# Kernel tuning notes

Hardware: AMD Instinct MI355X
Metric: run time of the kernel (lower is better)

The kernel has to match this reference:

```python
import jax, jax.numpy as jnp
import numpy as np

B, S, D, H = 2, 2048, 1024, 16
DK = D // H

def setup_inputs() -> dict:
    key = jax.random.key(0)
    ks = jax.random.split(key, 12)
    sc = 0.02
    return {
        "q": jax.random.normal(ks[0], (B, S, D), jnp.float32),
        "k": jax.random.normal(ks[1], (B, S, D), jnp.float32),
        "v": jax.random.normal(ks[2], (B, S, D), jnp.float32),
        "mask": jnp.ones((1, 1, S, S), jnp.int32),
        "w_q": jax.random.normal(ks[3], (D, D), jnp.float32) * sc,
        "b_q": jnp.zeros((D,), jnp.float32),
        "w_k": jax.random.normal(ks[4], (D, D), jnp.float32) * sc,
        "b_k": jnp.zeros((D,), jnp.float32),
        "w_v": jax.random.normal(ks[5], (D, D), jnp.float32) * sc,
        "b_v": jnp.zeros((D,), jnp.float32),
        "w_o": jax.random.normal(ks[6], (D, D), jnp.float32) * sc,
        "b_o": jnp.zeros((D,), jnp.float32),
    }

def reference(q, k, v, mask, w_q, b_q, w_k, b_k, w_v, b_v, w_o, b_o):
    # torch Linear: y = x @ W.T + b, W is [out, in]
    def lin(x, w, b):
        return jnp.einsum('bsd,ed->bse', x, w) + b
    # project and split heads -> [B, H, S, DK]
    def heads(x):
        return x.reshape(B, S, H, DK).transpose(0, 2, 1, 3)
    Q = heads(lin(q, w_q, b_q))
    K = heads(lin(k, w_k, b_k))
    V = heads(lin(v, w_v, b_v))
    scores = jnp.einsum('bhqd,bhkd->bhqk', Q, K) / jnp.sqrt(jnp.float32(DK))
    scores = jnp.where(mask == 0, jnp.float32(-1e9), scores)
    attn = jax.nn.softmax(scores, axis=-1)  # dropout p=0 -> identity
    ctx = jnp.einsum('bhqk,bhkd->bhqd', attn, V)
    ctx = ctx.transpose(0, 2, 1, 3).reshape(B, S, D)
    return lin(ctx, w_o, b_o)
```

## Files before the change

### kernel.cpp

```cpp
#include <hip/hip_runtime.h>
#include <stdint.h>


#define S_LEN 2048
#define LOG2E 1.4426950408889634f

using bf16x8 = __attribute__((ext_vector_type(8))) __bf16;
using f32x4 = __attribute__((ext_vector_type(4))) float;
using f32x16 = __attribute__((ext_vector_type(16))) float;
using u32x4 = __attribute__((ext_vector_type(4))) unsigned int;

__device__ __forceinline__ unsigned short f2bf(float x) {
  unsigned int u = __builtin_bit_cast(unsigned int, x);
  u += 0x7fffu + ((u >> 16) & 1u);
  return (unsigned short)(u >> 16);
}

__device__ __forceinline__ float bf2f(unsigned short u) {
  unsigned int x = ((unsigned int)u) << 16;
  return __builtin_bit_cast(float, x);
}

__device__ __forceinline__ void gload_lds16(const void* g, void* l) {
  __builtin_amdgcn_global_load_lds(
      (const __attribute__((address_space(1))) void*)g,
      (__attribute__((address_space(3))) void*)l, 16, 0, 0);
}

__device__ __forceinline__ unsigned int cvtpk(float lo, float hi) {
  unsigned int r;
  asm("v_cvt_pk_bf16_f32 %0, %1, %2" : "=v"(r) : "v"(lo), "v"(hi));
  return r;
}

__device__ __forceinline__ bf16x8 mkfrag(float p0, float p1, float p2, float p3,
                                         float p4, float p5, float p6, float p7) {
  auto r02 = __builtin_amdgcn_permlane32_swap(cvtpk(p0, p1), cvtpk(p4, p5),
                                              false, false);
  auto r13 = __builtin_amdgcn_permlane32_swap(cvtpk(p2, p3), cvtpk(p6, p7),
                                              false, false);
  u32x4 w = {(unsigned int)r02[0], (unsigned int)r13[0], (unsigned int)r02[1],
             (unsigned int)r13[1]};
  return __builtin_bit_cast(bf16x8, w);
}

__global__ void cvt7_kernel(const float* __restrict__ q,
                            const float* __restrict__ k,
                            const float* __restrict__ v,
                            const float* __restrict__ w0,
                            const float* __restrict__ w1,
                            const float* __restrict__ w2,
                            const float* __restrict__ w3,
                            unsigned short* __restrict__ dq,
                            unsigned short* __restrict__ dk,
                            unsigned short* __restrict__ dv,
                            unsigned short* __restrict__ e0,
                            unsigned short* __restrict__ e1,
                            unsigned short* __restrict__ e2,
                            unsigned short* __restrict__ e3) {
  const int y = blockIdx.y;
  const float* src;
  unsigned short* dst;
  int n4;
  if (y < 3) {
    src = y == 0 ? q : y == 1 ? k : v;
    dst = y == 0 ? dq : y == 1 ? dk : dv;
    n4 = 1048576;
  } else {
    int j = y - 3;
    src = j == 0 ? w0 : j == 1 ? w1 : j == 2 ? w2 : w3;
    dst = j == 0 ? e0 : j == 1 ? e1 : j == 2 ? e2 : e3;
    n4 = 262144;
  }
  int i = blockIdx.x * blockDim.x + threadIdx.x;
  int stride = gridDim.x * blockDim.x;
  for (; i < n4; i += stride) {
    float4 a = ((const float4*)src)[i];
    ushort4 o;
    o.x = f2bf(a.x);
    o.y = f2bf(a.y);
    o.z = f2bf(a.z);
    o.w = f2bf(a.w);
    ((ushort4*)dst)[i] = o;
  }
}

template <int OMODE>
__device__ __forceinline__ void qkv128_body(
    unsigned short* As, unsigned short* Bs,
    const unsigned short* __restrict__ X, const unsigned short* __restrict__ W,
    const float* __restrict__ bias, unsigned short* __restrict__ dst,
    float scale, int tx, int ty) {
  const int tid = threadIdx.x;
  const int wid = tid >> 6, lane = tid & 63;
  const int l15 = lane & 15, lg = lane >> 4;
  const int bm = ty * 128, bn = tx * 128;
  const int wr = (wid >> 1) * 64, wc = (wid & 1) * 64;

  const f32x4 fz = {0.f, 0.f, 0.f, 0.f};
  f32x4 acc[4][4];
#pragma unroll
  for (int m = 0; m < 4; ++m)
#pragma unroll
    for (int n = 0; n < 4; ++n) acc[m][n] = fz;

  const int srow = lane >> 2;
  const int scolz = ((lane & 3) ^ ((lane >> 3) & 3)) * 8;
  const int rcol = (lg ^ ((l15 >> 1) & 3)) * 8;

  for (int kt = 0; kt < 1024; kt += 32) {
#pragma unroll
    for (int c = 0; c < 2; ++c) {
      int ch = wid * 2 + c;
      gload_lds16(X + (size_t)(bm + ch * 16 + srow) * 1024 + kt + scolz,
                  As + ch * 512);
      gload_lds16(W + (size_t)(bn + ch * 16 + srow) * 1024 + kt + scolz,
                  Bs + ch * 512);
    }
    __syncthreads();

    bf16x8 af[4], bf[4];
#pragma unroll
    for (int m = 0; m < 4; ++m)
      af[m] = *(const bf16x8*)&As[(wr + m * 16 + l15) * 32 + rcol];
#pragma unroll
    for (int n = 0; n < 4; ++n)
      bf[n] = *(const bf16x8*)&Bs[(wc + n * 16 + l15) * 32 + rcol];

#pragma unroll
    for (int m = 0; m < 4; ++m)
#pragma unroll
      for (int n = 0; n < 4; ++n) {
        if (OMODE == 2)
          acc[m][n] = __builtin_amdgcn_mfma_f32_16x16x32_bf16(bf[n], af[m],
                                                              acc[m][n], 0, 0, 0);
        else
          acc[m][n] = __builtin_amdgcn_mfma_f32_16x16x32_bf16(af[m], bf[n],
                                                              acc[m][n], 0, 0, 0);
      }
    __syncthreads();
  }

#pragma unroll
  for (int m = 0; m < 4; ++m)
#pragma unroll
    for (int n = 0; n < 4; ++n)
#pragma unroll
      for (int j = 0; j < 4; ++j) {
        float a = acc[m][n][j];
        if (OMODE == 2) {
          int gn = bn + wc + n * 16 + lg * 4 + j;
          int gm = bm + wr + m * 16 + l15;
          float v = a + bias[gn];
          int b = gm >> 11, s = gm & 2047;
          int h = gn >> 6, dk = gn & 63;
          dst[(((size_t)(b * 16 + h)) * 64 + dk) * 2048 + s] = f2bf(v);
        } else {
          int gm = bm + wr + m * 16 + lg * 4 + j;
          int gn = bn + wc + n * 16 + l15;
          float v = (a + bias[gn]) * scale;
          int b = gm >> 11, s = gm & 2047;
          int h = gn >> 6, dk = gn & 63;
          dst[(((size_t)(b * 16 + h)) * 2048 + s) * 64 + dk] = f2bf(v);
        }
      }
}

__global__ __launch_bounds__(256) void gemm_qkv(
    const unsigned short* __restrict__ X0, const unsigned short* __restrict__ X1,
    const unsigned short* __restrict__ X2, const unsigned short* __restrict__ W0,
    const unsigned short* __restrict__ W1,
    const unsigned short* __restrict__ W2, const float* __restrict__ b0,
    const float* __restrict__ b1, const float* __restrict__ b2,
    unsigned short* __restrict__ dq, unsigned short* __restrict__ dk,
    unsigned short* __restrict__ dv) {
  __shared__ unsigned short As[128 * 32];
  __shared__ unsigned short Bs[128 * 32];
  const int lin = blockIdx.x + 8 * (blockIdx.y + 32 * blockIdx.z);
  const int xcd = lin & 7, v = lin >> 3;
  const int panel = xcd * 12 + (v >> 3);
  const int tx = v & 7;
  const int z = panel >> 5, ty = panel & 31;
  if (z == 0)
    qkv128_body<0>(As, Bs, X0, W0, b0, dq, 0.125f * LOG2E, tx, ty);
  else if (z == 1)
    qkv128_body<0>(As, Bs, X1, W1, b1, dk, 1.0f, tx, ty);
  else
    qkv128_body<2>(As, Bs, X2, W2, b2, dv, 1.0f, tx, ty);
}

__global__ __launch_bounds__(256) void gemm_out(
    const unsigned short* __restrict__ X, const unsigned short* __restrict__ W,
    const float* __restrict__ bias, float* __restrict__ dstF) {
  const int lin = blockIdx.x + 8 * blockIdx.y;
  const int xcd = lin & 7, v = lin >> 3;
  const int ty = xcd * 8 + (v >> 3);
  const int tx = v & 7;

  __shared__ unsigned short As[3][64 * 32];
  __shared__ unsigned short Bs[3][128 * 32];
  const int tid = threadIdx.x;
  const int wid = tid >> 6, lane = tid & 63;
  const int l15 = lane & 15, lg = lane >> 4;
  const int bm = ty * 64, bn = tx * 128;
  const int wr = (wid >> 1) * 32, wc = (wid & 1) * 64;

  const f32x4 fz = {0.f, 0.f, 0.f, 0.f};
  f32x4 acc[2][4];
#pragma unroll
  for (int m = 0; m < 2; ++m)
#pragma unroll
    for (int n = 0; n < 4; ++n) acc[m][n] = fz;

  const int srow = lane >> 2;
  const int scolz = ((lane & 3) ^ ((lane >> 3) & 3)) * 8;
  const int rcol = (lg ^ ((l15 >> 1) & 3)) * 8;

#define GSTAGE(buf, kt)                                                       \
  {                                                                           \
    gload_lds16(X + (size_t)(bm + wid * 16 + srow) * 1024 + (kt) + scolz,     \
                &As[buf][wid * 512]);                                         \
    _Pragma("unroll") for (int c = 0; c < 2; ++c) {                           \
      int ch = wid * 2 + c;                                                   \
      gload_lds16(W + (size_t)(bn + ch * 16 + srow) * 1024 + (kt) + scolz,    \
                  &Bs[buf][ch * 512]);                                        \
    }                                                                         \
  }

  GSTAGE(0, 0)
  GSTAGE(1, 32)
  int cur = 0;

  for (int it = 0; it < 32; ++it) {
    if (it < 31) {
      asm volatile("s_waitcnt vmcnt(3)\n\ts_barrier" ::: "memory");
    } else {
      asm volatile("s_waitcnt vmcnt(0)\n\ts_barrier" ::: "memory");
    }
    if (it < 30) {
      int nb = cur >= 1 ? cur - 1 : cur + 2;
      GSTAGE(nb, (it + 2) * 32)
    }

    bf16x8 af[2], bf[4];
#pragma unroll
    for (int m = 0; m < 2; ++m)
      af[m] = *(const bf16x8*)&As[cur][(wr + m * 16 + l15) * 32 + rcol];
#pragma unroll
    for (int n = 0; n < 4; ++n)
      bf[n] = *(const bf16x8*)&Bs[cur][(wc + n * 16 + l15) * 32 + rcol];

#pragma unroll
    for (int m = 0; m < 2; ++m)
#pragma unroll
      for (int n = 0; n < 4; ++n)
        acc[m][n] = __builtin_amdgcn_mfma_f32_16x16x32_bf16(af[m], bf[n],
                                                            acc[m][n], 0, 0, 0);
    cur = cur == 2 ? 0 : cur + 1;
  }
#undef GSTAGE

#pragma unroll
  for (int m = 0; m < 2; ++m)
#pragma unroll
    for (int n = 0; n < 4; ++n)
#pragma unroll
      for (int j = 0; j < 4; ++j) {
        int gm = bm + wr + m * 16 + lg * 4 + j;
        int gn = bn + wc + n * 16 + l15;
        dstF[(size_t)gm * 1024 + gn] = acc[m][n][j] + bias[gn];
      }
}

__global__ __launch_bounds__(256) void attn_kernel(
    const unsigned short* __restrict__ Q,
    const unsigned short* __restrict__ K,
    const unsigned short* __restrict__ VT,
    unsigned short* __restrict__ Opart, float* __restrict__ lvec) {
  const int orig = blockIdx.x;
  const int idx = (orig & 7) * 128 + (orig >> 3);
  const int bh = idx >> 5;
  const int u = idx & 31;
  const int qb = u >> 1;
  const int sp = u & 1;
  const int kt0 = sp * 1024;
  const int tid = threadIdx.x;
  const int w = tid >> 6;
  const int lane = tid & 63;
  const int l31 = lane & 31;
  const int hi = lane >> 5;
  const int q0 = qb * 128 + w * 32;

  __shared__ __align__(16) unsigned short Ks[2][64][64];
  __shared__ __align__(16) unsigned short Vs[2][64][64];

  const unsigned short* Qg = Q + ((size_t)bh * S_LEN + q0) * 64;
  const unsigned short* Kg = K + (size_t)bh * S_LEN * 64;
  const unsigned short* Vg = VT + (size_t)bh * 64 * S_LEN;

  bf16x8 qf[4];
#pragma unroll
  for (int kc = 0; kc < 4; ++kc)
    qf[kc] = *(const bf16x8*)&Qg[l31 * 64 + kc * 16 + hi * 8];

  const u32x4 ow = {0x3F803F80u, 0x3F803F80u, 0x3F803F80u, 0x3F803F80u};
  const bf16x8 onesf = __builtin_bit_cast(bf16x8, ow);

  const int srow = lane >> 3;
  const int sslot = (lane & 7) ^ srow;

#define STAGE_K(buf, kt)                                                      \
  {                                                                           \
    gload_lds16(Kg + ((size_t)((kt) + w * 16 + srow)) * 64 + sslot * 8,       \
                &Ks[buf][w * 16][0]);                                         \
    gload_lds16(Kg + ((size_t)((kt) + w * 16 + 8 + srow)) * 64 + sslot * 8,   \
                &Ks[buf][w * 16 + 8][0]);                                     \
  }
#define STAGE_V(buf, kt)                                                       \
  {                                                                            \
    gload_lds16(Vg + ((size_t)(w * 16 + srow)) * S_LEN + (kt) + sslot * 8,     \
                &Vs[buf][w * 16][0]);                                          \
    gload_lds16(Vg + ((size_t)(w * 16 + 8 + srow)) * S_LEN + (kt) + sslot * 8, \
                &Vs[buf][w * 16 + 8][0]);                                      \
  }

  const f32x16 fz16 = {};
  f32x16 O0 = {}, O1 = {}, Lacc = {};
  f32x16 sA0, sA1, sB0, sB1;

  STAGE_K(0, kt0)
  STAGE_V(0, kt0)
  STAGE_K(1, kt0 + 64)
  asm volatile("s_waitcnt vmcnt(2)\n\ts_barrier" ::: "memory");
  sA0 = fz16;
  sA1 = fz16;
  __builtin_amdgcn_s_setprio(1);
#pragma unroll
  for (int kc = 0; kc < 4; ++kc) {
    const int col = ((kc * 2 + hi) ^ (l31 & 7)) * 8;
    bf16x8 kf0 = *(const bf16x8*)&Ks[0][l31][col];
    bf16x8 kf1 = *(const bf16x8*)&Ks[0][32 + l31][col];
    sA0 = __builtin_amdgcn_mfma_f32_32x32x16_bf16(kf0, qf[kc], sA0, 0, 0, 0);
    sA1 = __builtin_amdgcn_mfma_f32_32x32x16_bf16(kf1, qf[kc], sA1, 0, 0, 0);
  }
  __builtin_amdgcn_s_setprio(0);
  STAGE_V(1, kt0 + 64)

#define BODY(T, SP0, SP1, SN0, SN1, PB, DO_PRE, DO_QK)                         \
  {                                                                            \
    if (DO_QK) {                                                               \
      asm volatile("s_waitcnt vmcnt(2)\n\ts_barrier" ::: "memory");            \
    } else {                                                                   \
      asm volatile("s_waitcnt vmcnt(0)\n\ts_barrier" ::: "memory");            \
    }                                                                          \
    if (DO_PRE) STAGE_K(PB, kt0 + ((T) + 2) * 64)                              \
    if (DO_QK) {                                                               \
      SN0 = fz16;                                                              \
      SN1 = fz16;                                                              \
      __builtin_amdgcn_s_setprio(1);                                           \
      _Pragma("unroll") for (int kc = 0; kc < 4; ++kc) {                       \
        const int col = ((kc * 2 + hi) ^ (l31 & 7)) * 8;                       \
        bf16x8 kf0 = *(const bf16x8*)&Ks[1 - (PB)][l31][col];                  \
        bf16x8 kf1 = *(const bf16x8*)&Ks[1 - (PB)][32 + l31][col];             \
        SN0 =                                                                  \
            __builtin_amdgcn_mfma_f32_32x32x16_bf16(kf0, qf[kc], SN0, 0, 0, 0);\
        SN1 =                                                                  \
            __builtin_amdgcn_mfma_f32_32x32x16_bf16(kf1, qf[kc], SN1, 0, 0, 0);\
      }                                                                        \
      __builtin_amdgcn_s_setprio(0);                                           \
    }                                                                          \
    _Pragma("unroll") for (int r = 0; r < 16; ++r) {                           \
      SP0[r] = exp2f(SP0[r]);                                                  \
      SP1[r] = exp2f(SP1[r]);                                                  \
    }                                                                          \
    {                                                                          \
      bf16x8 pa0 = mkfrag(SP0[0], SP0[1], SP0[2], SP0[3], SP0[4], SP0[5],      \
                          SP0[6], SP0[7]);                                     \
      bf16x8 pa1 = mkfrag(SP0[8], SP0[9], SP0[10], SP0[11], SP0[12], SP0[13],  \
                          SP0[14], SP0[15]);                                   \
      bf16x8 pa2 = mkfrag(SP1[0], SP1[1], SP1[2], SP1[3], SP1[4], SP1[5],      \
                          SP1[6], SP1[7]);                                     \
      bf16x8 pa3 = mkfrag(SP1[8], SP1[9], SP1[10], SP1[11], SP1[12], SP1[13],  \
                          SP1[14], SP1[15]);                                   \
      __builtin_amdgcn_s_setprio(1);                                           \
      _Pragma("unroll") for (int kc = 0; kc < 4; ++kc) {                       \
        const int col = ((kc * 2 + hi) ^ (l31 & 7)) * 8;                       \
        bf16x8 v0 = *(const bf16x8*)&Vs[PB][l31][col];                         \
        bf16x8 v1 = *(const bf16x8*)&Vs[PB][32 + l31][col];                    \
        bf16x8 pa = (kc == 0) ? pa0 : (kc == 1) ? pa1 : (kc == 2) ? pa2 : pa3; \
        O0 = __builtin_amdgcn_mfma_f32_32x32x16_bf16(pa, v0, O0, 0, 0, 0);     \
        O1 = __builtin_amdgcn_mfma_f32_32x32x16_bf16(pa, v1, O1, 0, 0, 0);     \
        Lacc = __builtin_amdgcn_mfma_f32_32x32x16_bf16(pa, onesf, Lacc, 0, 0,  \
                                                       0);                     \
      }                                                                        \
      __builtin_amdgcn_s_setprio(0);                                           \
    }                                                                          \
    asm volatile("s_barrier" ::: "memory");                                    \
    if (DO_PRE) STAGE_V(PB, kt0 + ((T) + 2) * 64)                              \
  }

  for (int tt = 0; tt < 7; ++tt) {
    const int te = 2 * tt;
    BODY(te, sA0, sA1, sB0, sB1, 0, 1, 1)
    BODY(te + 1, sB0, sB1, sA0, sA1, 1, 1, 1)
  }
  BODY(14, sA0, sA1, sB0, sB1, 0, 0, 1)
  BODY(15, sB0, sB1, sA0, sA1, 1, 0, 0)
#undef BODY
#undef STAGE_K
#undef STAGE_V

  const size_t rowbase = (size_t)(sp * 32 + bh) * 2048 + q0;
  if (l31 == 0) {
#pragma unroll
    for (int r = 0; r < 16; ++r) {
      int qr = (r & 3) + 8 * (r >> 2) + 4 * hi;
      lvec[rowbase + qr] = Lacc[r];
    }
  }
#pragma unroll
  for (int r = 0; r < 16; ++r) {
    int qr = (r & 3) + 8 * (r >> 2) + 4 * hi;
    float inv = __builtin_amdgcn_rcpf(Lacc[r]);
    size_t base = (rowbase + qr) * 64;
    Opart[base + l31] = f2bf(O0[r] * inv);
    Opart[base + 32 + l31] = f2bf(O1[r] * inv);
  }
}

__global__ __launch_bounds__(256) void combine_kernel(
    const unsigned short* __restrict__ Op, const float* __restrict__ lvec,
    unsigned short* __restrict__ CTX) {
  const int idx = blockIdx.x * 256 + threadIdx.x;
  const int row = idx >> 3;
  const int d0 = (idx & 7) * 8;
  const float l1 = lvec[row];
  const float l2 = lvec[65536 + row];
  const float inv = 1.0f / (l1 + l2);
  const float w1 = l1 * inv, w2 = l2 * inv;
  const size_t SPLIT = (size_t)32 * 2048 * 64;
  ushort4 vv1[2], vv2[2];
  vv1[0] = *(const ushort4*)&Op[(size_t)row * 64 + d0];
  vv1[1] = *(const ushort4*)&Op[(size_t)row * 64 + d0 + 4];
  vv2[0] = *(const ushort4*)&Op[SPLIT + (size_t)row * 64 + d0];
  vv2[1] = *(const ushort4*)&Op[SPLIT + (size_t)row * 64 + d0 + 4];
  const unsigned short* q1 = (const unsigned short*)vv1;
  const unsigned short* q2 = (const unsigned short*)vv2;
  unsigned short o8[8];
#pragma unroll
  for (int j = 0; j < 8; ++j)
    o8[j] = f2bf(w1 * bf2f(q1[j]) + w2 * bf2f(q2[j]));
  const int bh = row >> 11, s = row & 2047;
  const int b = bh >> 4, h = bh & 15;
  size_t o = ((size_t)(b * 2048 + s)) * 1024 + h * 64 + d0;
  *(u32x4*)&CTX[o] = *(const u32x4*)o8;
}

extern "C" void kernel_launch(void* const* d_in, const int* in_sizes, int n_in,
                              void* d_out, int out_size, void* d_ws,
                              size_t ws_size, hipStream_t stream) {
  const float* q = (const float*)d_in[0];
  const float* k = (const float*)d_in[1];
  const float* v = (const float*)d_in[2];
  const float* wq = (const float*)d_in[4];
  const float* bq = (const float*)d_in[5];
  const float* wk = (const float*)d_in[6];
  const float* bk = (const float*)d_in[7];
  const float* wv = (const float*)d_in[8];
  const float* bv = (const float*)d_in[9];
  const float* wo = (const float*)d_in[10];
  const float* bo = (const float*)d_in[11];
  float* out = (float*)d_out;

  const size_t NTOK = 4096 * 1024;
  unsigned short* ws = (unsigned short*)d_ws;
  unsigned short* xq = ws;
  unsigned short* xk = xq + NTOK;
  unsigned short* xv = xk + NTOK;
  unsigned short* wqb = xv + NTOK;
  unsigned short* wkb = wqb + 1048576;
  unsigned short* wvb = wkb + 1048576;
  unsigned short* wob = wvb + 1048576;
  unsigned short* Qp = wob + 1048576;
  unsigned short* Kp = Qp + NTOK;
  unsigned short* Vt = Kp + NTOK;
  unsigned short* Opart = ws;
  float* lvec = (float*)(ws + 8388608);
  unsigned short* CTX = Qp;

  cvt7_kernel<<<dim3(512, 7), 256, 0, stream>>>(q, k, v, wq, wk, wv, wo, xq, xk,
                                                xv, wqb, wkb, wvb, wob);

  gemm_qkv<<<dim3(8, 32, 3), 256, 0, stream>>>(xq, xk, xv, wqb, wkb, wvb, bq,
                                               bk, bv, Qp, Kp, Vt);

  attn_kernel<<<1024, 256, 0, stream>>>(Qp, Kp, Vt, Opart, lvec);

  combine_kernel<<<2048, 256, 0, stream>>>(Opart, lvec, CTX);

  gemm_out<<<dim3(8, 64), 256, 0, stream>>>(CTX, wob, bo, out);
}
```

Before: 148.2 us.

## Triple-buffer LDS tiles in QKV GEMM with async prefetch two stages ahead

The QKV projection GEMM now keeps three LDS buffers for the A and B tiles and issues the direct-to-LDS global loads two K-steps ahead. A single barrier per iteration with a partial vmcnt wait replaces the two __syncthreads. This is meant to hide global load latency behind the MFMA work. In exchange it triples the LDS footprint to 48KB per block, which may reduce occupancy.

```diff
diff --git a/kernel.cpp b/kernel.cpp
--- a/kernel.cpp
+++ b/kernel.cpp
@@ -87,7 +87,7 @@
 
 template <int OMODE>
 __device__ __forceinline__ void qkv128_body(
-    unsigned short* As, unsigned short* Bs,
+    unsigned short (*As)[4096], unsigned short (*Bs)[4096],
     const unsigned short* __restrict__ X, const unsigned short* __restrict__ W,
     const float* __restrict__ bias, unsigned short* __restrict__ dst,
     float scale, int tx, int ty) {
@@ -108,24 +108,39 @@
   const int scolz = ((lane & 3) ^ ((lane >> 3) & 3)) * 8;
   const int rcol = (lg ^ ((l15 >> 1) & 3)) * 8;
 
-  for (int kt = 0; kt < 1024; kt += 32) {
-#pragma unroll
-    for (int c = 0; c < 2; ++c) {
-      int ch = wid * 2 + c;
-      gload_lds16(X + (size_t)(bm + ch * 16 + srow) * 1024 + kt + scolz,
-                  As + ch * 512);
-      gload_lds16(W + (size_t)(bn + ch * 16 + srow) * 1024 + kt + scolz,
-                  Bs + ch * 512);
+#define GS(buf, kt)                                                           \
+  {                                                                           \
+    _Pragma("unroll") for (int c = 0; c < 2; ++c) {                           \
+      int ch = wid * 2 + c;                                                   \
+      gload_lds16(X + (size_t)(bm + ch * 16 + srow) * 1024 + (kt) + scolz,    \
+                  &As[buf][ch * 512]);                                        \
+      gload_lds16(W + (size_t)(bn + ch * 16 + srow) * 1024 + (kt) + scolz,    \
+                  &Bs[buf][ch * 512]);                                        \
+    }                                                                         \
+  }
+
+  GS(0, 0)
+  GS(1, 32)
+  int cur = 0;
+
+  for (int it = 0; it < 32; ++it) {
+    if (it < 31) {
+      asm volatile("s_waitcnt vmcnt(4)\n\ts_barrier" ::: "memory");
+    } else {
+      asm volatile("s_waitcnt vmcnt(0)\n\ts_barrier" ::: "memory");
     }
-    __syncthreads();
+    if (it < 30) {
+      int nb = cur >= 1 ? cur - 1 : cur + 2;
+      GS(nb, (it + 2) * 32)
+    }
 
     bf16x8 af[4], bf[4];
 #pragma unroll
     for (int m = 0; m < 4; ++m)
-      af[m] = *(const bf16x8*)&As[(wr + m * 16 + l15) * 32 + rcol];
+      af[m] = *(const bf16x8*)&As[cur][(wr + m * 16 + l15) * 32 + rcol];
 #pragma unroll
     for (int n = 0; n < 4; ++n)
-      bf[n] = *(const bf16x8*)&Bs[(wc + n * 16 + l15) * 32 + rcol];
+      bf[n] = *(const bf16x8*)&Bs[cur][(wc + n * 16 + l15) * 32 + rcol];
 
 #pragma unroll
     for (int m = 0; m < 4; ++m)
@@ -138,8 +153,9 @@
           acc[m][n] = __builtin_amdgcn_mfma_f32_16x16x32_bf16(af[m], bf[n],
                                                               acc[m][n], 0, 0, 0);
       }
-    __syncthreads();
-  }
+    cur = cur == 2 ? 0 : cur + 1;
+  }
+#undef GS
 
 #pragma unroll
   for (int m = 0; m < 4; ++m)
@@ -174,8 +190,8 @@
     const float* __restrict__ b1, const float* __restrict__ b2,
     unsigned short* __restrict__ dq, unsigned short* __restrict__ dk,
     unsigned short* __restrict__ dv) {
-  __shared__ unsigned short As[128 * 32];
-  __shared__ unsigned short Bs[128 * 32];
+  __shared__ unsigned short As[3][4096];
+  __shared__ unsigned short Bs[3][4096];
   const int lin = blockIdx.x + 8 * (blockIdx.y + 32 * blockIdx.z);
   const int xcd = lin & 7, v = lin >> 3;
   const int panel = xcd * 12 + (v >> 3);
```

New measurement: 157.9 us. 1.07x slower.
